# Optimization experiments

Measured on AMD Instinct MI355X. Metric: run time of the kernel, lower is better.

## Reference

```python
import jax, jax.numpy as jnp
import numpy as np

B, T, D, H = 8, 8192, 1024, 16
HD = D // H  # head_dim = 64


def setup_inputs() -> dict:
    key = jax.random.key(0)
    ks = jax.random.split(key, 6)
    x = jax.random.normal(ks[0], (B, D), jnp.float32)
    past_k = jax.random.normal(ks[1], (B, T, H, HD), jnp.float32)
    past_v = jax.random.normal(ks[2], (B, T, H, HD), jnp.float32)
    idx = jax.random.randint(ks[3], (B,), 0, T)
    W_attn = jax.random.normal(ks[4], (D, 3 * D), jnp.float32) * 0.02
    b_attn = jnp.zeros((3 * D,), jnp.float32)
    W_proj = jax.random.normal(ks[5], (D, D), jnp.float32) * 0.02
    b_proj = jnp.zeros((D,), jnp.float32)
    return dict(x=x, past_k=past_k, past_v=past_v, idx=idx,
                W_attn=W_attn, b_attn=b_attn, W_proj=W_proj, b_proj=b_proj)


def reference(x, past_k, past_v, idx, W_attn, b_attn, W_proj, b_proj):
    # fused qkv projection: [B, 3D]
    qkv = x @ W_attn + b_attn
    q, k, v = jnp.split(qkv, 3, axis=-1)
    q = q.reshape(B, 1, H, HD)          # q_len = 1 (decode step)
    k_step = k.reshape(B, H, HD)
    v_step = v.reshape(B, H, HD)
    # one-hot scatter update of KV cache at position idx (as in original)
    oh = jax.nn.one_hot(idx, T, dtype=x.dtype)[:, :, None, None]  # [B,T,1,1]
    k_all = past_k * (1.0 - oh) + oh * k_step[:, None]            # [B,T,H,HD]
    v_all = past_v * (1.0 - oh) + oh * v_step[:, None]
    # causal mask over cache: positions <= idx are valid
    mask = jnp.arange(T) <= idx[:, None]                          # [B,T]
    scale = 1.0 / jnp.sqrt(jnp.asarray(HD, x.dtype))
    scores = jnp.einsum('bqhd,bkhd->bhqk', q * scale, k_all)      # [B,H,1,T]
    big_neg = jnp.finfo(scores.dtype).min
    scores = jnp.where(mask[:, None, None, :], scores, big_neg)
    attn = jax.nn.softmax(scores, axis=-1)
    y = jnp.einsum('bhqk,bkhd->bqhd', attn, v_all).reshape(B, D)
    y = y @ W_proj + b_proj
    return (y, k_step, v_step)
```

## Files before the change

### kernel.cpp

```cpp
#include <hip/hip_runtime.h>
#include <hip/hip_bf16.h>

#define BB 8
#define TT 8192
#define HH 16
#define HDIM 64
#define DDIM 1024
#define NS 8
#define TSPLIT 1024

__device__ __forceinline__ int load_idx(const int* __restrict__ idx, int b) {
  const bool wide = (idx[1] == 0) && (idx[3] == 0) && (idx[5] == 0) && (idx[7] == 0);
  int v = wide ? idx[2 * b] : idx[b];
  return min(max(v, 0), TT - 1);
}

__global__ __launch_bounds__(256) void qkv_kernel(
    const float* __restrict__ x, const float* __restrict__ W,
    const float* __restrict__ bias,
    float* __restrict__ q_ws, float* __restrict__ kstep_ws,
    float* __restrict__ vstep_ws, float* __restrict__ out)
{
  __shared__ float x_s[DDIM];
  const int tid = threadIdx.x;
  const int g = blockIdx.x * 256 + tid;
  const int b = g / 3072;
  const int j = g % 3072;

  const float* xrow = x + b * DDIM;
  for (int i = tid; i < DDIM; i += 256) x_s[i] = xrow[i];
  __syncthreads();

  const float* wp = W + j;
  float a0 = 0.f, a1 = 0.f, a2 = 0.f, a3 = 0.f;
  #pragma unroll 4
  for (int dd = 0; dd < DDIM; dd += 4) {
    a0 += x_s[dd + 0] * wp[(size_t)(dd + 0) * 3072];
    a1 += x_s[dd + 1] * wp[(size_t)(dd + 1) * 3072];
    a2 += x_s[dd + 2] * wp[(size_t)(dd + 2) * 3072];
    a3 += x_s[dd + 3] * wp[(size_t)(dd + 3) * 3072];
  }
  float acc = (a0 + a1) + (a2 + a3) + bias[j];

  if (j < 1024) {
    q_ws[b * DDIM + j] = acc * 0.125f;
  } else if (j < 2048) {
    int jj = j - 1024;
    kstep_ws[b * DDIM + jj] = acc;
    out[8192 + b * DDIM + jj] = acc;
  } else {
    int jj = j - 2048;
    vstep_ws[b * DDIM + jj] = acc;
    out[16384 + b * DDIM + jj] = acc;
  }
}

__global__ __launch_bounds__(256) void attn_partial_kernel(
    const float* __restrict__ past_k, const float* __restrict__ past_v,
    const int* __restrict__ idx,
    const float* __restrict__ q_ws, const float* __restrict__ kstep_ws,
    const float* __restrict__ vstep_ws,
    float* __restrict__ part_m, float* __restrict__ part_l,
    float* __restrict__ part_o)
{
  const int tid = threadIdx.x;
  const int s  = blockIdx.x & (NS - 1);
  const int h  = (blockIdx.x >> 3) & (HH - 1);
  const int b  = blockIdx.x >> 7;
  const int idxb = load_idx(idx, b);
  const int t0 = s * TSPLIT;
  const int bhs = (b * HH + h) * NS + s;

  if (t0 > idxb) {
    if (tid == 0) { part_m[bhs] = -1e30f; part_l[bhs] = 0.f; }
    return;
  }
  const int nvalid = min(TSPLIT, idxb - t0 + 1);

  __shared__ float q_s[HDIM];
  __shared__ float p_s[TSPLIT];
  __shared__ float red_s[256];
  __shared__ float o_s[16 * HDIM];

  if (tid < HDIM) q_s[tid] = q_ws[b * DDIM + h * HDIM + tid];
  __syncthreads();

  float sc[4];
  const float* Kb = past_k + (((size_t)b * TT + t0) * HH + h) * HDIM;
  #pragma unroll
  for (int i = 0; i < 4; ++i) {
    const int tl = tid + i * 256;
    float v;
    if (tl >= nvalid) {
      v = -1e30f;
    } else if (t0 + tl == idxb) {
      const float* kr = kstep_ws + b * DDIM + h * HDIM;
      float acc = 0.f;
      #pragma unroll
      for (int d = 0; d < HDIM; ++d) acc += q_s[d] * kr[d];
      v = acc;
    } else {
      const float4* kr = (const float4*)(Kb + (size_t)tl * (HH * HDIM));
      float a0 = 0.f, a1 = 0.f, a2 = 0.f, a3 = 0.f;
      #pragma unroll
      for (int seg = 0; seg < 16; ++seg) {
        float4 u = kr[seg];
        a0 += q_s[seg * 4 + 0] * u.x;
        a1 += q_s[seg * 4 + 1] * u.y;
        a2 += q_s[seg * 4 + 2] * u.z;
        a3 += q_s[seg * 4 + 3] * u.w;
      }
      v = (a0 + a1) + (a2 + a3);
    }
    sc[i] = v;
  }

  float lmax = fmaxf(fmaxf(sc[0], sc[1]), fmaxf(sc[2], sc[3]));
  red_s[tid] = lmax;
  __syncthreads();
  for (int st = 128; st > 0; st >>= 1) {
    if (tid < st) red_s[tid] = fmaxf(red_s[tid], red_s[tid + st]);
    __syncthreads();
  }
  const float mh = red_s[0];
  __syncthreads();

  float lsum = 0.f;
  #pragma unroll
  for (int i = 0; i < 4; ++i) {
    float p = __expf(sc[i] - mh);
    p_s[tid + i * 256] = p;
    lsum += p;
  }
  red_s[tid] = lsum;
  __syncthreads();
  for (int st = 128; st > 0; st >>= 1) {
    if (tid < st) red_s[tid] += red_s[tid + st];
    __syncthreads();
  }
  if (tid == 0) { part_m[bhs] = mh; part_l[bhs] = red_s[0]; }

  const int tg = tid >> 4;
  const int d0 = (tid & 15) * 4;
  float a0 = 0.f, a1 = 0.f, a2 = 0.f, a3 = 0.f;
  const float* Vb = past_v + (((size_t)b * TT + t0) * HH + h) * HDIM;
  for (int tl = tg; tl < nvalid; tl += 16) {
    const float p = p_s[tl];
    if (t0 + tl == idxb) {
      const float* vr = vstep_ws + b * DDIM + h * HDIM + d0;
      a0 += p * vr[0]; a1 += p * vr[1]; a2 += p * vr[2]; a3 += p * vr[3];
    } else {
      const float4 u = *(const float4*)(Vb + (size_t)tl * (HH * HDIM) + d0);
      a0 += p * u.x; a1 += p * u.y; a2 += p * u.z; a3 += p * u.w;
    }
  }
  o_s[tg * HDIM + d0 + 0] = a0;
  o_s[tg * HDIM + d0 + 1] = a1;
  o_s[tg * HDIM + d0 + 2] = a2;
  o_s[tg * HDIM + d0 + 3] = a3;
  __syncthreads();
  if (tid < HDIM) {
    float acc = 0.f;
    #pragma unroll
    for (int g2 = 0; g2 < 16; ++g2) acc += o_s[g2 * HDIM + tid];
    part_o[(size_t)bhs * HDIM + tid] = acc;
  }
}

__global__ __launch_bounds__(64) void attn_combine_kernel(
    const float* __restrict__ part_m, const float* __restrict__ part_l,
    const float* __restrict__ part_o, float* __restrict__ y_ws)
{
  const int bh = blockIdx.x;
  const int lane = threadIdx.x;

  float m[NS], l[NS];
  float M = -1e30f;
  #pragma unroll
  for (int s = 0; s < NS; ++s) {
    m[s] = part_m[bh * NS + s];
    l[s] = part_l[bh * NS + s];
    M = fmaxf(M, m[s]);
  }
  float L = 0.f, acc = 0.f;
  #pragma unroll
  for (int s = 0; s < NS; ++s) {
    float w = (l[s] > 0.f) ? __expf(m[s] - M) : 0.f;
    if (w > 0.f) {
      L += l[s] * w;
      acc += w * part_o[(size_t)(bh * NS + s) * HDIM + lane];
    }
  }
  y_ws[bh * HDIM + lane] = (L > 0.f) ? (acc / L) : 0.f;
}

__global__ __launch_bounds__(256) void proj_kernel(
    const float* __restrict__ y_ws, const float* __restrict__ W,
    const float* __restrict__ bias, float* __restrict__ out)
{
  __shared__ float y_s[DDIM];
  const int tid = threadIdx.x;
  const int g = blockIdx.x * 256 + tid;
  const int b = g >> 10;
  const int j = g & 1023;

  const float* yrow = y_ws + b * DDIM;
  for (int i = tid; i < DDIM; i += 256) y_s[i] = yrow[i];
  __syncthreads();

  const float* wp = W + j;
  float a0 = 0.f, a1 = 0.f, a2 = 0.f, a3 = 0.f;
  #pragma unroll 4
  for (int dd = 0; dd < DDIM; dd += 4) {
    a0 += y_s[dd + 0] * wp[(size_t)(dd + 0) * DDIM];
    a1 += y_s[dd + 1] * wp[(size_t)(dd + 1) * DDIM];
    a2 += y_s[dd + 2] * wp[(size_t)(dd + 2) * DDIM];
    a3 += y_s[dd + 3] * wp[(size_t)(dd + 3) * DDIM];
  }
  float acc = (a0 + a1) + (a2 + a3) + bias[j];
  out[b * DDIM + j] = acc;
}

extern "C" void kernel_launch(void* const* d_in, const int* in_sizes, int n_in,
                              void* d_out, int out_size, void* d_ws, size_t ws_size,
                              hipStream_t stream) {
  const float* x      = (const float*)d_in[0];
  const float* past_k = (const float*)d_in[1];
  const float* past_v = (const float*)d_in[2];
  const int*   idx    = (const int*)  d_in[3];
  const float* W_attn = (const float*)d_in[4];
  const float* b_attn = (const float*)d_in[5];
  const float* W_proj = (const float*)d_in[6];
  const float* b_proj = (const float*)d_in[7];
  float* out = (float*)d_out;

  float* ws       = (float*)d_ws;
  float* q_ws     = ws;
  float* kstep_ws = ws + 8192;
  float* vstep_ws = ws + 16384;
  float* y_ws     = ws + 24576;
  float* part_m   = ws + 32768;
  float* part_l   = ws + 33792;
  float* part_o   = ws + 34816;

  qkv_kernel<<<dim3(96), dim3(256), 0, stream>>>(
      x, W_attn, b_attn, q_ws, kstep_ws, vstep_ws, out);
  attn_partial_kernel<<<dim3(BB * HH * NS), dim3(256), 0, stream>>>(
      past_k, past_v, idx, q_ws, kstep_ws, vstep_ws, part_m, part_l, part_o);
  attn_combine_kernel<<<dim3(BB * HH), dim3(64), 0, stream>>>(
      part_m, part_l, part_o, y_ws);
  proj_kernel<<<dim3(32), dim3(256), 0, stream>>>(
      y_ws, W_proj, b_proj, out);
}
```

Baseline: 604.3 us.

## Split-K the QKV and output projections and double attention sequence splits

Both GEMV projections move from a few blocks that each loop over all of D to split-K kernels with float4 weight loads, followed by separate reduce kernels. The goal is more parallelism, since the original qkv used 96 blocks and proj used 32. Attention now splits T into 16 chunks of 512 instead of 8 of 1024, and the shared-memory tree reductions become wavefront shuffle reductions. The cost is two extra launches and partial-sum workspace traffic. Because W is re-read once per batch row, weight bandwidth is multiplied by B.

```diff
diff --git a/kernel.cpp b/kernel.cpp
--- a/kernel.cpp
+++ b/kernel.cpp
@@ -6,8 +6,10 @@
 #define HH 16
 #define HDIM 64
 #define DDIM 1024
-#define NS 8
-#define TSPLIT 1024
+#define NS 16
+#define TSPLIT 512
+#define KS1 16
+#define KS2 32
 
 __device__ __forceinline__ int load_idx(const int* __restrict__ idx, int b) {
   const bool wide = (idx[1] == 0) && (idx[3] == 0) && (idx[5] == 0) && (idx[7] == 0);
@@ -15,41 +17,53 @@
   return min(max(v, 0), TT - 1);
 }
 
-__global__ __launch_bounds__(256) void qkv_kernel(
+__global__ __launch_bounds__(256) void qkv_split_kernel(
     const float* __restrict__ x, const float* __restrict__ W,
-    const float* __restrict__ bias,
+    float* __restrict__ part)
+{
+  const int bid = blockIdx.x;
+  const int ks = bid & (KS1 - 1);
+  const int jc = (bid >> 4) % 3;
+  const int b  = bid / (3 * KS1);
+  const int tid = threadIdx.x;
+
+  __shared__ float x_s[64];
+  if (tid < 64) x_s[tid] = x[b * DDIM + ks * 64 + tid];
+  __syncthreads();
+
+  const int j0 = jc * 1024 + tid * 4;
+  const float* wp = W + (size_t)(ks * 64) * 3072 + j0;
+  float4 acc = {0.f, 0.f, 0.f, 0.f};
+  #pragma unroll 8
+  for (int dd = 0; dd < 64; ++dd) {
+    float4 w4 = *(const float4*)(wp + (size_t)dd * 3072);
+    const float xv = x_s[dd];
+    acc.x += xv * w4.x; acc.y += xv * w4.y;
+    acc.z += xv * w4.z; acc.w += xv * w4.w;
+  }
+  *(float4*)(part + (size_t)ks * (BB * 3072) + b * 3072 + j0) = acc;
+}
+
+__global__ __launch_bounds__(256) void qkv_reduce_kernel(
+    const float* __restrict__ part, const float* __restrict__ bias,
     float* __restrict__ q_ws, float* __restrict__ kstep_ws,
     float* __restrict__ vstep_ws, float* __restrict__ out)
 {
-  __shared__ float x_s[DDIM];
-  const int tid = threadIdx.x;
-  const int g = blockIdx.x * 256 + tid;
+  const int g = blockIdx.x * 256 + threadIdx.x;
   const int b = g / 3072;
   const int j = g % 3072;
-
-  const float* xrow = x + b * DDIM;
-  for (int i = tid; i < DDIM; i += 256) x_s[i] = xrow[i];
-  __syncthreads();
-
-  const float* wp = W + j;
-  float a0 = 0.f, a1 = 0.f, a2 = 0.f, a3 = 0.f;
-  #pragma unroll 4
-  for (int dd = 0; dd < DDIM; dd += 4) {
-    a0 += x_s[dd + 0] * wp[(size_t)(dd + 0) * 3072];
-    a1 += x_s[dd + 1] * wp[(size_t)(dd + 1) * 3072];
-    a2 += x_s[dd + 2] * wp[(size_t)(dd + 2) * 3072];
-    a3 += x_s[dd + 3] * wp[(size_t)(dd + 3) * 3072];
-  }
-  float acc = (a0 + a1) + (a2 + a3) + bias[j];
+  float acc = bias[j];
+  #pragma unroll
+  for (int ks = 0; ks < KS1; ++ks) acc += part[(size_t)ks * (BB * 3072) + g];
 
   if (j < 1024) {
     q_ws[b * DDIM + j] = acc * 0.125f;
   } else if (j < 2048) {
-    int jj = j - 1024;
+    const int jj = j - 1024;
     kstep_ws[b * DDIM + jj] = acc;
     out[8192 + b * DDIM + jj] = acc;
   } else {
-    int jj = j - 2048;
+    const int jj = j - 2048;
     vstep_ws[b * DDIM + jj] = acc;
     out[16384 + b * DDIM + jj] = acc;
   }
@@ -65,8 +79,8 @@
 {
   const int tid = threadIdx.x;
   const int s  = blockIdx.x & (NS - 1);
-  const int h  = (blockIdx.x >> 3) & (HH - 1);
-  const int b  = blockIdx.x >> 7;
+  const int h  = (blockIdx.x >> 4) & (HH - 1);
+  const int b  = blockIdx.x >> 8;
   const int idxb = load_idx(idx, b);
   const int t0 = s * TSPLIT;
   const int bhs = (b * HH + h) * NS + s;
@@ -79,32 +93,27 @@
 
   __shared__ float q_s[HDIM];
   __shared__ float p_s[TSPLIT];
-  __shared__ float red_s[256];
+  __shared__ float redm[8], redl[8];
   __shared__ float o_s[16 * HDIM];
 
   if (tid < HDIM) q_s[tid] = q_ws[b * DDIM + h * HDIM + tid];
   __syncthreads();
 
-  float sc[4];
   const float* Kb = past_k + (((size_t)b * TT + t0) * HH + h) * HDIM;
-  #pragma unroll
-  for (int i = 0; i < 4; ++i) {
+  const float* krow_step = kstep_ws + b * DDIM + h * HDIM;
+  float sc[2];
+  #pragma unroll
+  for (int i = 0; i < 2; ++i) {
     const int tl = tid + i * 256;
-    float v;
-    if (tl >= nvalid) {
-      v = -1e30f;
-    } else if (t0 + tl == idxb) {
-      const float* kr = kstep_ws + b * DDIM + h * HDIM;
-      float acc = 0.f;
-      #pragma unroll
-      for (int d = 0; d < HDIM; ++d) acc += q_s[d] * kr[d];
-      v = acc;
-    } else {
-      const float4* kr = (const float4*)(Kb + (size_t)tl * (HH * HDIM));
+    float v = -1e30f;
+    if (tl < nvalid) {
+      const float* kr = (t0 + tl == idxb) ? krow_step
+                                          : (Kb + (size_t)tl * (HH * HDIM));
+      const float4* k4 = (const float4*)kr;
       float a0 = 0.f, a1 = 0.f, a2 = 0.f, a3 = 0.f;
       #pragma unroll
       for (int seg = 0; seg < 16; ++seg) {
-        float4 u = kr[seg];
+        float4 u = k4[seg];
         a0 += q_s[seg * 4 + 0] * u.x;
         a1 += q_s[seg * 4 + 1] * u.y;
         a2 += q_s[seg * 4 + 2] * u.z;
@@ -115,44 +124,40 @@
     sc[i] = v;
   }
 
-  float lmax = fmaxf(fmaxf(sc[0], sc[1]), fmaxf(sc[2], sc[3]));
-  red_s[tid] = lmax;
-  __syncthreads();
-  for (int st = 128; st > 0; st >>= 1) {
-    if (tid < st) red_s[tid] = fmaxf(red_s[tid], red_s[tid + st]);
-    __syncthreads();
-  }
-  const float mh = red_s[0];
-  __syncthreads();
+  float lmax = fmaxf(sc[0], sc[1]);
+  #pragma unroll
+  for (int m = 32; m > 0; m >>= 1) lmax = fmaxf(lmax, __shfl_xor(lmax, m, 64));
+  if ((tid & 63) == 0) redm[tid >> 6] = lmax;
+  __syncthreads();
+  const float mh = fmaxf(fmaxf(redm[0], redm[1]), fmaxf(redm[2], redm[3]));
 
   float lsum = 0.f;
   #pragma unroll
-  for (int i = 0; i < 4; ++i) {
+  for (int i = 0; i < 2; ++i) {
     float p = __expf(sc[i] - mh);
     p_s[tid + i * 256] = p;
     lsum += p;
   }
-  red_s[tid] = lsum;
-  __syncthreads();
-  for (int st = 128; st > 0; st >>= 1) {
-    if (tid < st) red_s[tid] += red_s[tid + st];
-    __syncthreads();
-  }
-  if (tid == 0) { part_m[bhs] = mh; part_l[bhs] = red_s[0]; }
+  #pragma unroll
+  for (int m = 32; m > 0; m >>= 1) lsum += __shfl_xor(lsum, m, 64);
+  if ((tid & 63) == 0) redl[tid >> 6] = lsum;
+  __syncthreads();
+  if (tid == 0) {
+    part_m[bhs] = mh;
+    part_l[bhs] = redl[0] + redl[1] + redl[2] + redl[3];
+  }
 
   const int tg = tid >> 4;
   const int d0 = (tid & 15) * 4;
+  const float* Vb = past_v + (((size_t)b * TT + t0) * HH + h) * HDIM + d0;
+  const float* vrow_step = vstep_ws + b * DDIM + h * HDIM + d0;
   float a0 = 0.f, a1 = 0.f, a2 = 0.f, a3 = 0.f;
-  const float* Vb = past_v + (((size_t)b * TT + t0) * HH + h) * HDIM;
   for (int tl = tg; tl < nvalid; tl += 16) {
     const float p = p_s[tl];
-    if (t0 + tl == idxb) {
-      const float* vr = vstep_ws + b * DDIM + h * HDIM + d0;
-      a0 += p * vr[0]; a1 += p * vr[1]; a2 += p * vr[2]; a3 += p * vr[3];
-    } else {
-      const float4 u = *(const float4*)(Vb + (size_t)tl * (HH * HDIM) + d0);
-      a0 += p * u.x; a1 += p * u.y; a2 += p * u.z; a3 += p * u.w;
-    }
+    const float4 u = *(const float4*)((t0 + tl == idxb)
+                                          ? vrow_step
+                                          : (Vb + (size_t)tl * (HH * HDIM)));
+    a0 += p * u.x; a1 += p * u.y; a2 += p * u.z; a3 += p * u.w;
   }
   o_s[tg * HDIM + d0 + 0] = a0;
   o_s[tg * HDIM + d0 + 1] = a1;
@@ -194,31 +199,42 @@
   y_ws[bh * HDIM + lane] = (L > 0.f) ? (acc / L) : 0.f;
 }
 
-__global__ __launch_bounds__(256) void proj_kernel(
+__global__ __launch_bounds__(256) void proj_split_kernel(
     const float* __restrict__ y_ws, const float* __restrict__ W,
-    const float* __restrict__ bias, float* __restrict__ out)
-{
-  __shared__ float y_s[DDIM];
+    float* __restrict__ part)
+{
+  const int bid = blockIdx.x;
+  const int ks = bid & (KS2 - 1);
+  const int b  = bid >> 5;
   const int tid = threadIdx.x;
-  const int g = blockIdx.x * 256 + tid;
-  const int b = g >> 10;
+
+  __shared__ float y_s[32];
+  if (tid < 32) y_s[tid] = y_ws[b * DDIM + ks * 32 + tid];
+  __syncthreads();
+
+  const int j0 = tid * 4;
+  const float* wp = W + (size_t)(ks * 32) * DDIM + j0;
+  float4 acc = {0.f, 0.f, 0.f, 0.f};
+  #pragma unroll 8
+  for (int dd = 0; dd < 32; ++dd) {
+    float4 w4 = *(const float4*)(wp + (size_t)dd * DDIM);
+    const float yv = y_s[dd];
+    acc.x += yv * w4.x; acc.y += yv * w4.y;
+    acc.z += yv * w4.z; acc.w += yv * w4.w;
+  }
+  *(float4*)(part + (size_t)ks * (BB * DDIM) + b * DDIM + j0) = acc;
+}
+
+__global__ __launch_bounds__(256) void proj_reduce_kernel(
+    const float* __restrict__ part, const float* __restrict__ bias,
+    float* __restrict__ out)
+{
+  const int g = blockIdx.x * 256 + threadIdx.x;
   const int j = g & 1023;
-
-  const float* yrow = y_ws + b * DDIM;
-  for (int i = tid; i < DDIM; i += 256) y_s[i] = yrow[i];
-  __syncthreads();
-
-  const float* wp = W + j;
-  float a0 = 0.f, a1 = 0.f, a2 = 0.f, a3 = 0.f;
-  #pragma unroll 4
-  for (int dd = 0; dd < DDIM; dd += 4) {
-    a0 += y_s[dd + 0] * wp[(size_t)(dd + 0) * DDIM];
-    a1 += y_s[dd + 1] * wp[(size_t)(dd + 1) * DDIM];
-    a2 += y_s[dd + 2] * wp[(size_t)(dd + 2) * DDIM];
-    a3 += y_s[dd + 3] * wp[(size_t)(dd + 3) * DDIM];
-  }
-  float acc = (a0 + a1) + (a2 + a3) + bias[j];
-  out[b * DDIM + j] = acc;
+  float acc = bias[j];
+  #pragma unroll
+  for (int ks = 0; ks < KS2; ++ks) acc += part[(size_t)ks * (BB * DDIM) + g];
+  out[g] = acc;
 }
 
 extern "C" void kernel_launch(void* const* d_in, const int* in_sizes, int n_in,
@@ -234,21 +250,27 @@
   const float* b_proj = (const float*)d_in[7];
   float* out = (float*)d_out;
 
-  float* ws       = (float*)d_ws;
-  float* q_ws     = ws;
-  float* kstep_ws = ws + 8192;
-  float* vstep_ws = ws + 16384;
-  float* y_ws     = ws + 24576;
-  float* part_m   = ws + 32768;
-  float* part_l   = ws + 33792;
-  float* part_o   = ws + 34816;
-
-  qkv_kernel<<<dim3(96), dim3(256), 0, stream>>>(
-      x, W_attn, b_attn, q_ws, kstep_ws, vstep_ws, out);
+  float* ws        = (float*)d_ws;
+  float* q_ws      = ws;
+  float* kstep_ws  = ws + 8192;
+  float* vstep_ws  = ws + 16384;
+  float* y_ws      = ws + 24576;
+  float* part_m    = ws + 32768;
+  float* part_l    = ws + 34816;
+  float* part_o    = ws + 36864;
+  float* qkv_part  = ws + 167936;
+  float* proj_part = ws + 561152;
+
+  qkv_split_kernel<<<dim3(BB * 3 * KS1), dim3(256), 0, stream>>>(
+      x, W_attn, qkv_part);
+  qkv_reduce_kernel<<<dim3(96), dim3(256), 0, stream>>>(
+      qkv_part, b_attn, q_ws, kstep_ws, vstep_ws, out);
   attn_partial_kernel<<<dim3(BB * HH * NS), dim3(256), 0, stream>>>(
       past_k, past_v, idx, q_ws, kstep_ws, vstep_ws, part_m, part_l, part_o);
   attn_combine_kernel<<<dim3(BB * HH), dim3(64), 0, stream>>>(
       part_m, part_l, part_o, y_ws);
-  proj_kernel<<<dim3(32), dim3(256), 0, stream>>>(
-      y_ws, W_proj, b_proj, out);
-}
+  proj_split_kernel<<<dim3(BB * KS2), dim3(256), 0, stream>>>(
+      y_ws, W_proj, proj_part);
+  proj_reduce_kernel<<<dim3(32), dim3(256), 0, stream>>>(
+      proj_part, b_proj, out);
+}
```

Result: faster. 540.2 us (-10.6%).
